# Performance work log

Measured on AMD Instinct MI355X. Metric: run time of the kernel, lower is better.

## Reference

```python
import jax, jax.numpy as jnp
import numpy as np
from jax import lax

START_IDX = 510
END_IDX = 511
SEQ_LEN = 32768
NUM_TAGS = 512
NEG_FILL = -10000.0


def setup_inputs() -> dict:
    key = jax.random.key(0)
    k1, k2 = jax.random.split(key)
    unary = jax.random.normal(k1, (SEQ_LEN, 1, NUM_TAGS), dtype=jnp.float32)
    trans = jax.random.normal(k2, (1, NUM_TAGS, NUM_TAGS), dtype=jnp.float32)
    lengths = jnp.full((1,), SEQ_LEN, dtype=jnp.int64)
    return {"unary": unary, "trans": trans, "lengths": lengths}


def reference(unary, trans, lengths):
    # unary: [T, 1, N] -> [T, N]; trans: [1, N, N] -> [N, N], trans[j, k] = score(k -> j)
    u = unary[:, 0, :]
    tr = trans[0]
    n_tags = tr.shape[0]

    # alphas[start_idx] = 0, else -10000
    alphas0 = jnp.where(jnp.arange(n_tags) == START_IDX,
                        jnp.float32(0.0), jnp.float32(NEG_FILL))

    def step(alphas, u_t):
        scores = alphas[None, :] + tr          # [N, N]: to-tag j, from-tag k
        best = jnp.argmax(scores, axis=1)      # backpointers [N]
        vit = jnp.max(scores, axis=1)          # [N]
        return vit + u_t, best

    alphas, backptrs = lax.scan(step, alphas0, u)   # backptrs: [T, N] int

    terminal = alphas + tr[END_IDX, :]
    best_tag = jnp.argmax(terminal)
    path_score = terminal[best_tag]

    # traceback: tag_{t-1} = backptrs[t][tag_t]
    def tb(tag, bp_t):
        return bp_t[tag], tag

    _, path = lax.scan(tb, best_tag, backptrs, reverse=True)  # [T]
    return path[:, None], path_score
```

## Files before the change

kernel.cpp:

```cpp
#include <hip/hip_runtime.h>
#include <cstdint>
#include <cstddef>

#define SEQ       32768
#define NT        512
#define START_TAG 510
#define END_TAG   511
#define NEGF      -10000.0f
#define KCH       64
#define NCH       (SEQ / KCH)

#define NBLK      64
#define TPB       256
#define CPB       8

#define BP_BYTES  ((size_t)SEQ * NT * sizeof(unsigned short))
#define M_OFF     (BP_BYTES)
#define M_BYTES   ((size_t)NCH * NT * sizeof(unsigned short))
#define BD_OFF    (M_OFF + M_BYTES)
#define BD_BYTES  ((size_t)NCH * sizeof(int))
#define AG_OFF    ((BD_OFF + BD_BYTES + 63) & ~(size_t)63)

__global__ __launch_bounds__(NT) void init_k(unsigned long long* AgP) {
    const int t = threadIdx.x;
    const float a0 = (t == START_TAG) ? 0.0f : NEGF;
    AgP[t]      = (unsigned long long)__float_as_uint(a0);
    AgP[NT + t] = ((unsigned long long)0xFFFFFFFFu << 32)
                | (unsigned long long)__float_as_uint(NEGF);
}

__global__ __launch_bounds__(TPB) void viterbi_fwd(const float* __restrict__ u,
                                                   const float* __restrict__ trans,
                                                   unsigned short* __restrict__ bp,
                                                   unsigned long long* AgP) {
    __shared__ float4 abuf[2][NT / 4];

    const int tid  = threadIdx.x;
    const int wv   = tid >> 6;
    const int lane = tid & 63;
    const int g    = lane >> 5;
    const int m    = lane & 31;
    const int b    = (int)blockIdx.x;
    const int j    = b * CPB + wv * 2 + g;
    const int i0   = 16 * m;

    float treg[16];
    #pragma unroll
    for (int k = 0; k < 16; ++k) treg[k] = trans[(size_t)j * NT + i0 + k];

    float uval = 0.0f;
    if (m == 0) uval = u[j];

    for (int t = 0; t < SEQ; ++t) {
        const int par = t & 1;

        float unext = 0.0f;
        const int tn = (t + 1 < SEQ) ? (t + 1) : t;
        if (m == 0) unext = u[(size_t)tn * NT + j];

        if (wv == 0) {
            const unsigned long long* sb = AgP + (size_t)par * NT + lane;
            unsigned long long va[8];
            const unsigned expt = (unsigned)t;
            for (;;) {
                bool ok = true;
                #pragma unroll
                for (int r = 0; r < 8; ++r) {
                    va[r] = __hip_atomic_load(&sb[r * 64], __ATOMIC_RELAXED,
                                              __HIP_MEMORY_SCOPE_AGENT);
                    ok &= ((unsigned)(va[r] >> 32) == expt);
                }
                if (ok) break;
                __builtin_amdgcn_s_sleep(1);
            }
            float* awf = (float*)&abuf[par][0];
            #pragma unroll
            for (int r = 0; r < 8; ++r) {
                const int i    = r * 64 + lane;
                const int phys = i ^ (((i >> 5) & 7) << 2);
                awf[phys] = __uint_as_float((unsigned)va[r]);
            }
        }
        __syncthreads();

        float cv[4]; int ci[4];
        #pragma unroll
        for (int kk = 0; kk < 4; ++kk) {
            const int ib = i0 + 4 * kk;
            const int pb = ib ^ (((ib >> 5) & 7) << 2);
            const float4 a4 = abuf[par][pb >> 2];
            float bv = a4.x + treg[4 * kk + 0]; int bi = ib;
            float s;
            s = a4.y + treg[4 * kk + 1]; if (s > bv) { bv = s; bi = ib + 1; }
            s = a4.z + treg[4 * kk + 2]; if (s > bv) { bv = s; bi = ib + 2; }
            s = a4.w + treg[4 * kk + 3]; if (s > bv) { bv = s; bi = ib + 3; }
            cv[kk] = bv; ci[kk] = bi;
        }
        float bv = cv[0]; int bi = ci[0];
        #pragma unroll
        for (int kk = 1; kk < 4; ++kk) {
            if (cv[kk] > bv) { bv = cv[kk]; bi = ci[kk]; }
        }

        #pragma unroll
        for (int h = 1; h <= 16; h <<= 1) {
            const float ov = __shfl_xor(bv, h);
            const int   oi = __shfl_xor(bi, h);
            if (ov > bv || (ov == bv && oi < bi)) { bv = ov; bi = oi; }
        }

        const int oi1 = __shfl(bi, 32);
        if (lane == 0) {
            *(unsigned*)&bp[(size_t)t * NT + b * CPB + wv * 2] =
                (unsigned)(bi & 0xFFFF) | ((unsigned)oi1 << 16);
        }

        if (m == 0) {
            const float na = bv + uval;
            const unsigned long long pk =
                ((unsigned long long)(unsigned)(t + 1) << 32)
                | (unsigned long long)__float_as_uint(na);
            __hip_atomic_store(&AgP[(size_t)((t + 1) & 1) * NT + j], pk,
                               __ATOMIC_RELAXED, __HIP_MEMORY_SCOPE_AGENT);
        }
        uval = unext;
    }
}

__global__ __launch_bounds__(NT) void mbuild_k(const unsigned short* __restrict__ bp,
                                               unsigned short* __restrict__ M) {
    __shared__ unsigned short R[2][NT];
    const int c = (int)blockIdx.x, j = threadIdx.x;
    const size_t base = (size_t)c * KCH * NT;
    R[0][j] = bp[base + j];
    int cb = 0;
    for (int t = 1; t < KCH; ++t) {
        const unsigned short r = bp[base + (size_t)t * NT + j];
        __syncthreads();
        R[cb ^ 1][j] = R[cb][r];
        cb ^= 1;
    }
    __syncthreads();
    M[(size_t)c * NT + j] = R[cb][j];
}

__global__ __launch_bounds__(NT) void chase_k(const unsigned long long* __restrict__ AgP,
                                              const float* __restrict__ tr,
                                              const unsigned short* __restrict__ M,
                                              int* __restrict__ boundary,
                                              float* __restrict__ out) {
    __shared__ float sv[NT];
    __shared__ int   si[NT];
    const int j = threadIdx.x;
    sv[j] = __uint_as_float((unsigned)AgP[j]) + tr[(size_t)END_TAG * NT + j];
    si[j] = j;
    __syncthreads();
    for (int off = NT / 2; off > 0; off >>= 1) {
        if (j < off) {
            const float a = sv[j], b = sv[j + off];
            if (b > a || (b == a && si[j + off] < si[j])) { sv[j] = b; si[j] = si[j + off]; }
        }
        __syncthreads();
    }
    if (j == 0) {
        out[SEQ] = sv[0];
        int tag = si[0];
        boundary[NCH - 1] = tag;
        for (int c = NCH - 1; c >= 1; --c) {
            tag = (int)M[(size_t)c * NT + tag];
            boundary[c - 1] = tag;
        }
    }
}

__global__ __launch_bounds__(64) void traceback_k(const unsigned short* __restrict__ bp,
                                                  const int* __restrict__ boundary,
                                                  float* __restrict__ out) {
    if (threadIdx.x != 0) return;
    const int c    = (int)blockIdx.x;
    int       tag  = boundary[c];
    const int tend = (c + 1) * KCH - 1;
    out[tend] = (float)tag;
    for (int t = tend - 1; t >= c * KCH; --t) {
        tag = (int)bp[(size_t)(t + 1) * NT + tag];
        out[t] = (float)tag;
    }
}

extern "C" void kernel_launch(void* const* d_in, const int* in_sizes, int n_in,
                              void* d_out, int out_size, void* d_ws, size_t ws_size,
                              hipStream_t stream) {
    const float* unary = (const float*)d_in[0];
    const float* trans = (const float*)d_in[1];
    float* out = (float*)d_out;
    char*  ws  = (char*)d_ws;

    unsigned short*     bp       = (unsigned short*)ws;
    unsigned short*     M        = (unsigned short*)(ws + M_OFF);
    int*                boundary = (int*)(ws + BD_OFF);
    unsigned long long* AgP      = (unsigned long long*)(ws + AG_OFF);
    (void)in_sizes; (void)n_in; (void)out_size; (void)ws_size;

    init_k<<<1, NT, 0, stream>>>(AgP);
    viterbi_fwd<<<NBLK, TPB, 0, stream>>>(unary, trans, bp, AgP);
    mbuild_k<<<NCH, NT, 0, stream>>>(bp, M);
    chase_k<<<1, NT, 0, stream>>>(AgP, trans, M, boundary, out);
    traceback_k<<<NCH, 64, 0, stream>>>(bp, boundary, out);
}
```

Measured before the change: 59.64 ms.

## Specialize a polling wave and consolidate the Viterbi forward pass into fewer blocks

The forward kernel is restructured so that wave 0 of each block only polls the global alpha vector and fills shared memory, while the remaining 8 waves compute maxima for 4 tags each. The grid shrinks from 64 to 16 blocks, which reduces the number of participants in the per-step cross-block handshake. The s_sleep in the spin loop is removed to cut polling latency. In exchange, each lane does twice as many candidate comparisons per step, and the busy-spinning polling wave adds memory traffic.

```diff
diff --git a/kernel.cpp b/kernel.cpp
--- a/kernel.cpp
+++ b/kernel.cpp
@@ -10,9 +10,9 @@
 #define KCH       64
 #define NCH       (SEQ / KCH)
 
-#define NBLK      64
-#define TPB       256
-#define CPB       8
+#define NBLK      16
+#define TPB       576
+#define CPB       32
 
 #define BP_BYTES  ((size_t)SEQ * NT * sizeof(unsigned short))
 #define M_OFF     (BP_BYTES)
@@ -38,27 +38,11 @@
     const int tid  = threadIdx.x;
     const int wv   = tid >> 6;
     const int lane = tid & 63;
-    const int g    = lane >> 5;
-    const int m    = lane & 31;
     const int b    = (int)blockIdx.x;
-    const int j    = b * CPB + wv * 2 + g;
-    const int i0   = 16 * m;
-
-    float treg[16];
-    #pragma unroll
-    for (int k = 0; k < 16; ++k) treg[k] = trans[(size_t)j * NT + i0 + k];
-
-    float uval = 0.0f;
-    if (m == 0) uval = u[j];
-
-    for (int t = 0; t < SEQ; ++t) {
-        const int par = t & 1;
-
-        float unext = 0.0f;
-        const int tn = (t + 1 < SEQ) ? (t + 1) : t;
-        if (m == 0) unext = u[(size_t)tn * NT + j];
-
-        if (wv == 0) {
+
+    if (wv == 0) {
+        for (int t = 0; t < SEQ; ++t) {
+            const int par = t & 1;
             const unsigned long long* sb = AgP + (size_t)par * NT + lane;
             unsigned long long va[8];
             const unsigned expt = (unsigned)t;
@@ -71,7 +55,6 @@
                     ok &= ((unsigned)(va[r] >> 32) == expt);
                 }
                 if (ok) break;
-                __builtin_amdgcn_s_sleep(1);
             }
             float* awf = (float*)&abuf[par][0];
             #pragma unroll
@@ -80,50 +63,80 @@
                 const int phys = i ^ (((i >> 5) & 7) << 2);
                 awf[phys] = __uint_as_float((unsigned)va[r]);
             }
-        }
-        __syncthreads();
-
-        float cv[4]; int ci[4];
+            __syncthreads();
+        }
+    } else {
+        const int cwv = wv - 1;
+        const int g   = lane >> 4;
+        const int m   = lane & 15;
+        const int j   = b * CPB + cwv * 4 + g;
+        const int i0  = 32 * m;
+
+        float4 treg[8];
         #pragma unroll
-        for (int kk = 0; kk < 4; ++kk) {
-            const int ib = i0 + 4 * kk;
-            const int pb = ib ^ (((ib >> 5) & 7) << 2);
-            const float4 a4 = abuf[par][pb >> 2];
-            float bv = a4.x + treg[4 * kk + 0]; int bi = ib;
-            float s;
-            s = a4.y + treg[4 * kk + 1]; if (s > bv) { bv = s; bi = ib + 1; }
-            s = a4.z + treg[4 * kk + 2]; if (s > bv) { bv = s; bi = ib + 2; }
-            s = a4.w + treg[4 * kk + 3]; if (s > bv) { bv = s; bi = ib + 3; }
-            cv[kk] = bv; ci[kk] = bi;
-        }
-        float bv = cv[0]; int bi = ci[0];
-        #pragma unroll
-        for (int kk = 1; kk < 4; ++kk) {
-            if (cv[kk] > bv) { bv = cv[kk]; bi = ci[kk]; }
-        }
-
-        #pragma unroll
-        for (int h = 1; h <= 16; h <<= 1) {
-            const float ov = __shfl_xor(bv, h);
-            const int   oi = __shfl_xor(bi, h);
-            if (ov > bv || (ov == bv && oi < bi)) { bv = ov; bi = oi; }
-        }
-
-        const int oi1 = __shfl(bi, 32);
-        if (lane == 0) {
-            *(unsigned*)&bp[(size_t)t * NT + b * CPB + wv * 2] =
-                (unsigned)(bi & 0xFFFF) | ((unsigned)oi1 << 16);
-        }
-
-        if (m == 0) {
-            const float na = bv + uval;
-            const unsigned long long pk =
-                ((unsigned long long)(unsigned)(t + 1) << 32)
-                | (unsigned long long)__float_as_uint(na);
-            __hip_atomic_store(&AgP[(size_t)((t + 1) & 1) * NT + j], pk,
-                               __ATOMIC_RELAXED, __HIP_MEMORY_SCOPE_AGENT);
-        }
-        uval = unext;
+        for (int q = 0; q < 8; ++q)
+            treg[q] = *(const float4*)&trans[(size_t)j * NT + i0 + 4 * q];
+
+        float uval = 0.0f;
+        if (m == 0) uval = u[j];
+
+        for (int t = 0; t < SEQ; ++t) {
+            const int par = t & 1;
+
+            float unext = 0.0f;
+            const int tn = (t + 1 < SEQ) ? (t + 1) : t;
+            if (m == 0) unext = u[(size_t)tn * NT + j];
+
+            __syncthreads();
+
+            float bv8[8]; int bi8[8];
+            #pragma unroll
+            for (int q = 0; q < 8; ++q) {
+                const int ib  = i0 + 4 * q;
+                const int f4i = ((ib >> 2) ^ (m & 7));
+                const float4 a4 = abuf[par][f4i];
+                const float4 tq = treg[q];
+                float bv = a4.x + tq.x; int bi = ib;
+                float s;
+                s = a4.y + tq.y; if (s > bv) { bv = s; bi = ib + 1; }
+                s = a4.z + tq.z; if (s > bv) { bv = s; bi = ib + 2; }
+                s = a4.w + tq.w; if (s > bv) { bv = s; bi = ib + 3; }
+                bv8[q] = bv; bi8[q] = bi;
+            }
+            #pragma unroll
+            for (int st = 1; st < 8; st <<= 1)
+                #pragma unroll
+                for (int q = 0; q < 8; q += 2 * st)
+                    if (bv8[q + st] > bv8[q]) { bv8[q] = bv8[q + st]; bi8[q] = bi8[q + st]; }
+            float bv = bv8[0]; int bi = bi8[0];
+
+            #pragma unroll
+            for (int h = 1; h <= 8; h <<= 1) {
+                const float ov = __shfl_xor(bv, h);
+                const int   oi = __shfl_xor(bi, h);
+                if (ov > bv || (ov == bv && oi < bi)) { bv = ov; bi = oi; }
+            }
+
+            if (m == 0) {
+                const float na = bv + uval;
+                const unsigned long long pk =
+                    ((unsigned long long)(unsigned)(t + 1) << 32)
+                    | (unsigned long long)__float_as_uint(na);
+                __hip_atomic_store(&AgP[(size_t)((t + 1) & 1) * NT + j], pk,
+                                   __ATOMIC_RELAXED, __HIP_MEMORY_SCOPE_AGENT);
+            }
+
+            const int r1 = __shfl(bi, 16);
+            const int r2 = __shfl(bi, 32);
+            const int r3 = __shfl(bi, 48);
+            if (lane == 0) {
+                uint2 pk2;
+                pk2.x = (unsigned)(bi & 0xFFFF) | ((unsigned)r1 << 16);
+                pk2.y = (unsigned)(r2 & 0xFFFF) | ((unsigned)r3 << 16);
+                *(uint2*)&bp[(size_t)t * NT + b * CPB + cwv * 4] = pk2;
+            }
+            uval = unext;
+        }
     }
 }
 
```

Result: slower. 78.68 ms (+31.9%).

## Use fewer larger blocks, drop poll sleep, publish alphas before backpointer store

Applied to the files above, without the earlier changes.

Cuts the forward grid from 64 blocks of 256 threads to 16 blocks of 1024 threads, so fewer blocks take part in the per-step cross-block handshake through global atomics. The spin-wait no longer sleeps between polls, and each step's alpha store now comes before the backpointer write, shortening the critical path between steps. Transition rows are loaded as float4 vectors and the max reduction becomes a tree. The trade-offs are heavier polling traffic on the shared flags and a larger __syncthreads barrier spanning 16 waves per block.

```diff
diff --git a/kernel.cpp b/kernel.cpp
--- a/kernel.cpp
+++ b/kernel.cpp
@@ -10,9 +10,9 @@
 #define KCH       64
 #define NCH       (SEQ / KCH)
 
-#define NBLK      64
-#define TPB       256
-#define CPB       8
+#define NBLK      16
+#define TPB       1024
+#define CPB       32
 
 #define BP_BYTES  ((size_t)SEQ * NT * sizeof(unsigned short))
 #define M_OFF     (BP_BYTES)
@@ -38,15 +38,17 @@
     const int tid  = threadIdx.x;
     const int wv   = tid >> 6;
     const int lane = tid & 63;
-    const int g    = lane >> 5;
+    const int gp   = lane >> 5;
     const int m    = lane & 31;
     const int b    = (int)blockIdx.x;
-    const int j    = b * CPB + wv * 2 + g;
+    const int jb   = b * CPB + wv * 2;
+    const int j    = jb + gp;
     const int i0   = 16 * m;
 
-    float treg[16];
-    #pragma unroll
-    for (int k = 0; k < 16; ++k) treg[k] = trans[(size_t)j * NT + i0 + k];
+    const float4 t0 = *(const float4*)&trans[(size_t)j * NT + i0];
+    const float4 t1 = *(const float4*)&trans[(size_t)j * NT + i0 + 4];
+    const float4 t2 = *(const float4*)&trans[(size_t)j * NT + i0 + 8];
+    const float4 t3 = *(const float4*)&trans[(size_t)j * NT + i0 + 12];
 
     float uval = 0.0f;
     if (m == 0) uval = u[j];
@@ -71,7 +73,6 @@
                     ok &= ((unsigned)(va[r] >> 32) == expt);
                 }
                 if (ok) break;
-                __builtin_amdgcn_s_sleep(1);
             }
             float* awf = (float*)&abuf[par][0];
             #pragma unroll
@@ -83,36 +84,41 @@
         }
         __syncthreads();
 
-        float cv[4]; int ci[4];
-        #pragma unroll
-        for (int kk = 0; kk < 4; ++kk) {
-            const int ib = i0 + 4 * kk;
-            const int pb = ib ^ (((ib >> 5) & 7) << 2);
-            const float4 a4 = abuf[par][pb >> 2];
-            float bv = a4.x + treg[4 * kk + 0]; int bi = ib;
-            float s;
-            s = a4.y + treg[4 * kk + 1]; if (s > bv) { bv = s; bi = ib + 1; }
-            s = a4.z + treg[4 * kk + 2]; if (s > bv) { bv = s; bi = ib + 2; }
-            s = a4.w + treg[4 * kk + 3]; if (s > bv) { bv = s; bi = ib + 3; }
-            cv[kk] = bv; ci[kk] = bi;
-        }
-        float bv = cv[0]; int bi = ci[0];
-        #pragma unroll
-        for (int kk = 1; kk < 4; ++kk) {
-            if (cv[kk] > bv) { bv = cv[kk]; bi = ci[kk]; }
-        }
+        float v0, v1, v2, v3; int x0, x1, x2, x3; float s;
+        {   const int ib = i0;      const int pb = ib ^ (((ib >> 5) & 7) << 2);
+            const float4 a = abuf[par][pb >> 2];
+            v0 = a.x + t0.x; x0 = ib;
+            s = a.y + t0.y; if (s > v0) { v0 = s; x0 = ib + 1; }
+            s = a.z + t0.z; if (s > v0) { v0 = s; x0 = ib + 2; }
+            s = a.w + t0.w; if (s > v0) { v0 = s; x0 = ib + 3; } }
+        {   const int ib = i0 + 4;  const int pb = ib ^ (((ib >> 5) & 7) << 2);
+            const float4 a = abuf[par][pb >> 2];
+            v1 = a.x + t1.x; x1 = ib;
+            s = a.y + t1.y; if (s > v1) { v1 = s; x1 = ib + 1; }
+            s = a.z + t1.z; if (s > v1) { v1 = s; x1 = ib + 2; }
+            s = a.w + t1.w; if (s > v1) { v1 = s; x1 = ib + 3; } }
+        {   const int ib = i0 + 8;  const int pb = ib ^ (((ib >> 5) & 7) << 2);
+            const float4 a = abuf[par][pb >> 2];
+            v2 = a.x + t2.x; x2 = ib;
+            s = a.y + t2.y; if (s > v2) { v2 = s; x2 = ib + 1; }
+            s = a.z + t2.z; if (s > v2) { v2 = s; x2 = ib + 2; }
+            s = a.w + t2.w; if (s > v2) { v2 = s; x2 = ib + 3; } }
+        {   const int ib = i0 + 12; const int pb = ib ^ (((ib >> 5) & 7) << 2);
+            const float4 a = abuf[par][pb >> 2];
+            v3 = a.x + t3.x; x3 = ib;
+            s = a.y + t3.y; if (s > v3) { v3 = s; x3 = ib + 1; }
+            s = a.z + t3.z; if (s > v3) { v3 = s; x3 = ib + 2; }
+            s = a.w + t3.w; if (s > v3) { v3 = s; x3 = ib + 3; } }
+        if (v1 > v0) { v0 = v1; x0 = x1; }
+        if (v3 > v2) { v2 = v3; x2 = x3; }
+        if (v2 > v0) { v0 = v2; x0 = x2; }
+        float bv = v0; int bi = x0;
 
         #pragma unroll
         for (int h = 1; h <= 16; h <<= 1) {
             const float ov = __shfl_xor(bv, h);
             const int   oi = __shfl_xor(bi, h);
             if (ov > bv || (ov == bv && oi < bi)) { bv = ov; bi = oi; }
-        }
-
-        const int oi1 = __shfl(bi, 32);
-        if (lane == 0) {
-            *(unsigned*)&bp[(size_t)t * NT + b * CPB + wv * 2] =
-                (unsigned)(bi & 0xFFFF) | ((unsigned)oi1 << 16);
         }
 
         if (m == 0) {
@@ -122,6 +128,12 @@
                 | (unsigned long long)__float_as_uint(na);
             __hip_atomic_store(&AgP[(size_t)((t + 1) & 1) * NT + j], pk,
                                __ATOMIC_RELAXED, __HIP_MEMORY_SCOPE_AGENT);
+        }
+
+        const int oi1 = __shfl(bi, 32);
+        if (lane == 0) {
+            *(unsigned*)&bp[(size_t)t * NT + jb] =
+                (unsigned)(bi & 0xFFFF) | ((unsigned)oi1 << 16);
         }
         uval = unext;
     }
```

After: 69.36 ms. 1.16x slower.
